# Kernel tuning notes

Hardware: AMD Instinct MI355X
Metric: run time of the kernel (lower is better)

## Reference

```python
import jax, jax.numpy as jnp
import numpy as np

B, S, HID, NH = 4, 1024, 1024, 16
HD = HID // NH  # 64


def setup_inputs() -> dict:
    key = jax.random.key(0)
    ks = jax.random.split(key, 8)
    scale = 0.02
    return {
        "attention_mask": jnp.zeros((B, 1, 1, S), dtype=jnp.float32),
        "query": jax.random.normal(ks[0], (B, S, HID), dtype=jnp.float32),
        "key": jax.random.normal(ks[1], (B, S, HID), dtype=jnp.float32),
        "value": jax.random.normal(ks[2], (B, S, HID), dtype=jnp.float32),
        "Wq": jax.random.normal(ks[3], (HID, HID), dtype=jnp.float32) * scale,
        "bq": jnp.zeros((HID,), dtype=jnp.float32),
        "Wk": jax.random.normal(ks[4], (HID, HID), dtype=jnp.float32) * scale,
        "bk": jnp.zeros((HID,), dtype=jnp.float32),
    }


def reference(attention_mask, query, key, value, Wq, bq, Wk, bk):
    # Linear projections (torch Linear: x @ W.T + b)
    q = query @ Wq.T + bq  # [B,S,HID]
    k = key @ Wk.T + bk    # [B,S,HID]
    # split heads -> [B,NH,S,HD]
    q = q.reshape(B, S, NH, HD).transpose(0, 2, 1, 3)
    k = k.reshape(B, S, NH, HD).transpose(0, 2, 1, 3)
    scores = jnp.einsum("bhqd,bhkd->bhqk", q, k) / jnp.sqrt(jnp.float32(HD))
    scores = scores + attention_mask  # additive mask broadcast [B,1,1,S]
    probs = jax.nn.softmax(scores, axis=-1)  # [B,NH,S,S]
    # V is shared across heads; head-mean folds into a single contraction:
    # mean_h(probs_h @ V) = (sum_h probs_h) @ V / NH
    out = jnp.einsum("bhqk,bkv->bqv", probs, value) / NH  # [B,S,HID]
    return out
```

## Files before the change

kernel.cpp:

```cpp
#include <hip/hip_runtime.h>
#include <hip/hip_bf16.h>
#include <hip/hip_fp16.h>

#define B_    4
#define S_    1024
#define HID_  1024
#define NH_   16
#define HD_   64

typedef _Float16 half8 __attribute__((ext_vector_type(8)));
typedef _Float16 half4v __attribute__((ext_vector_type(4)));
typedef float f32x4 __attribute__((ext_vector_type(4)));

#define LOG2E 1.44269504f

__device__ __forceinline__ void gload_lds16(const void* g, void* l) {
    __builtin_amdgcn_global_load_lds(
        (const __attribute__((address_space(1))) unsigned int*)g,
        (__attribute__((address_space(3))) unsigned int*)l, 16, 0, 0);
}

__global__ __launch_bounds__(256) void pack_qkw(
    const float* __restrict__ s0, _Float16* __restrict__ d0, int n40,
    const float* __restrict__ s1, _Float16* __restrict__ d1, int n41,
    const float* __restrict__ s2, _Float16* __restrict__ d2, int n42,
    const float* __restrict__ s3, _Float16* __restrict__ d3, int n43)
{
    int y = blockIdx.y;
    const float* s = y == 0 ? s0 : y == 1 ? s1 : y == 2 ? s2 : s3;
    _Float16*    d = y == 0 ? d0 : y == 1 ? d1 : y == 2 ? d2 : d3;
    int n4         = y == 0 ? n40 : y == 1 ? n41 : y == 2 ? n42 : n43;
    int i = blockIdx.x * 256 + threadIdx.x;
    if (i >= n4) return;
    float4 v = ((const float4*)s)[i];
    half4v h;
    h[0] = (_Float16)v.x; h[1] = (_Float16)v.y;
    h[2] = (_Float16)v.z; h[3] = (_Float16)v.w;
    ((half4v*)d)[i] = h;
}

__global__ __launch_bounds__(256) void vt_combine(
    const _Float16* __restrict__ P, _Float16* __restrict__ o,
    const float* __restrict__ V, _Float16* __restrict__ Vt)
{
    __shared__ float t[32][33];
    if (blockIdx.y == 0) {
        if (blockIdx.x >= 2048) return;
        const long QS = (long)B_ * S_ * S_;
        long i = (long)(blockIdx.x * 256 + threadIdx.x) * 8;
        half8 a = *(const half8*)(P + i);
        half8 b = *(const half8*)(P + QS + i);
        half8 c = *(const half8*)(P + 2 * QS + i);
        half8 d = *(const half8*)(P + 3 * QS + i);
        half8 r;
#pragma unroll
        for (int e = 0; e < 8; e++)
            r[e] = (_Float16)((float)a[e] + (float)b[e] + (float)c[e] + (float)d[e]);
        *(half8*)(o + i) = r;
    } else {
        const int x  = blockIdx.x;
        const int b  = x >> 10;
        const int s0 = ((x >> 5) & 31) * 32;
        const int h0 = (x & 31) * 32;
        const int tx = threadIdx.x & 31, ty = threadIdx.x >> 5;
#pragma unroll
        for (int rr = 0; rr < 4; rr++) {
            int s = s0 + ty + rr * 8;
            t[ty + rr * 8][tx] = V[((long)b * S_ + s) * HID_ + h0 + tx];
        }
        __syncthreads();
#pragma unroll
        for (int rr = 0; rr < 4; rr++) {
            int h = h0 + ty + rr * 8;
            Vt[((long)b * HID_ + h) * S_ + s0 + tx] = (_Float16)t[tx][ty + rr * 8];
        }
    }
}

__global__ __launch_bounds__(512) void proj_qk_f16(
    const _Float16* __restrict__ Aq, const _Float16* __restrict__ Wqh,
    const float* __restrict__ bq_, _Float16* __restrict__ Oq,
    const _Float16* __restrict__ Ak, const _Float16* __restrict__ Wkh,
    const float* __restrict__ bk_, _Float16* __restrict__ Ok)
{
    const _Float16* A  = blockIdx.z ? Ak : Aq;
    const _Float16* Bm = blockIdx.z ? Wkh : Wqh;
    const float* bias  = blockIdx.z ? bk_ : bq_;
    _Float16* Co       = blockIdx.z ? Ok : Oq;

    __shared__ _Float16 Al[128 * 32];
    __shared__ _Float16 Bl[128 * 32];

    const int tid  = threadIdx.x;
    const int wv   = tid >> 6;
    const int lane = tid & 63;
    const int l15  = lane & 15;
    const int quad = lane >> 4;
    const int wm   = wv & 1, wn = wv >> 1;
    const int m0   = blockIdx.y * 128, n0 = blockIdx.x * 128;
    const int sr   = tid >> 2;
    const int sc   = (tid & 3) * 8;

    f32x4 acc[4][2];
#pragma unroll
    for (int i = 0; i < 4; i++)
#pragma unroll
        for (int j = 0; j < 2; j++) acc[i][j] = (f32x4){0.f, 0.f, 0.f, 0.f};

    for (int kt = 0; kt < HID_; kt += 32) {
        gload_lds16(A  + (long)(m0 + sr) * HID_ + kt + sc, Al + (long)tid * 8);
        gload_lds16(Bm + (long)(n0 + sr) * HID_ + kt + sc, Bl + (long)tid * 8);
        __syncthreads();

        half8 af[4], bfm[2];
#pragma unroll
        for (int i = 0; i < 4; i++)
            af[i] = *(const half8*)(Al + (wm * 64 + i * 16 + l15) * 32 + quad * 8);
#pragma unroll
        for (int j = 0; j < 2; j++)
            bfm[j] = *(const half8*)(Bl + (wn * 32 + j * 16 + l15) * 32 + quad * 8);
#pragma unroll
        for (int i = 0; i < 4; i++)
#pragma unroll
            for (int j = 0; j < 2; j++)
                acc[i][j] = __builtin_amdgcn_mfma_f32_16x16x32_f16(
                    af[i], bfm[j], acc[i][j], 0, 0, 0);
        __syncthreads();
    }

#pragma unroll
    for (int j = 0; j < 2; j++) {
        int col = n0 + wn * 32 + j * 16 + l15;
        float bv = bias[col];
        int h = col >> 6, d = col & 63;
#pragma unroll
        for (int i = 0; i < 4; i++) {
            int row = m0 + wm * 64 + i * 16 + quad * 4;
            int bb = row >> 10, ss = row & 1023;
#pragma unroll
            for (int r = 0; r < 4; r++)
                Co[((long)(bb * NH_ + h) * S_ + ss + r) * HD_ + d] =
                    (_Float16)(acc[i][j][r] + bv);
        }
    }
}

__global__ __launch_bounds__(512) void attn_psum_f16(
    const _Float16* __restrict__ qb,
    const _Float16* __restrict__ kb,
    const float* __restrict__ mask,
    _Float16* __restrict__ P)
{
    const int b    = blockIdx.y;
    const int q0   = blockIdx.x * 16;
    const int hz   = blockIdx.z;
    const int tid  = threadIdx.x;
    const int w    = tid >> 6;
    const int lane = tid & 63;
    const int l15  = lane & 15;
    const int quad = lane >> 4;

    __shared__ float redS[2][16][8];

    const float SC = 0.125f * LOG2E;

    float mreg[8];
#pragma unroll
    for (int t = 0; t < 8; t++)
        mreg[t] = mask[b * S_ + t * 128 + w * 16 + l15] * LOG2E;

    f32x4 acc[8];
#pragma unroll
    for (int t = 0; t < 8; t++) acc[t] = (f32x4){0.f, 0.f, 0.f, 0.f};

    for (int ii = 0; ii < 4; ii++) {
        const int h = hz * 4 + ii;
        const _Float16* qh = qb + ((long)(b * NH_ + h) * S_) * HD_;
        const _Float16* kh = kb + ((long)(b * NH_ + h) * S_) * HD_;

        half8 a0 = *(const half8*)(qh + (long)(q0 + l15) * HD_ + quad * 8);
        half8 a1 = *(const half8*)(qh + (long)(q0 + l15) * HD_ + 32 + quad * 8);

        f32x4 s[8];
#pragma unroll
        for (int cc = 0; cc < 8; cc++) {
            const _Float16* kp =
                kh + (long)(cc * 128 + w * 16 + l15) * HD_ + quad * 8;
            half8 b0 = *(const half8*)kp;
            half8 b1 = *(const half8*)(kp + 32);
            f32x4 c = (f32x4){0.f, 0.f, 0.f, 0.f};
            c = __builtin_amdgcn_mfma_f32_16x16x32_f16(a0, b0, c, 0, 0, 0);
            c = __builtin_amdgcn_mfma_f32_16x16x32_f16(a1, b1, c, 0, 0, 0);
            s[cc] = c;
        }

        const int p = ii & 1;
        float sm[4] = {0.f, 0.f, 0.f, 0.f};
#pragma unroll
        for (int t = 0; t < 8; t++)
#pragma unroll
            for (int r = 0; r < 4; r++) {
                float pr = exp2f(s[t][r] * SC + mreg[t]);
                s[t][r] = pr;
                sm[r] += pr;
            }
#pragma unroll
        for (int off = 1; off < 16; off <<= 1)
#pragma unroll
            for (int r = 0; r < 4; r++) sm[r] += __shfl_xor(sm[r], off);
        if (l15 == 0)
#pragma unroll
            for (int r = 0; r < 4; r++) redS[p][quad * 4 + r][w] = sm[r];
        __syncthreads();

#pragma unroll
        for (int r = 0; r < 4; r++) {
            float4 v0 = *(float4*)&redS[p][quad * 4 + r][0];
            float4 v1 = *(float4*)&redS[p][quad * 4 + r][4];
            float tot = (v0.x + v0.y + v0.z + v0.w) + (v1.x + v1.y + v1.z + v1.w);
            float inv = 1.f / tot;
#pragma unroll
            for (int t = 0; t < 8; t++) acc[t][r] += s[t][r] * inv;
        }
    }

    _Float16* prow = P + (long)hz * ((long)B_ * S_ * S_) + (long)(b * S_ + q0) * S_;
#pragma unroll
    for (int t = 0; t < 8; t++)
#pragma unroll
        for (int r = 0; r < 4; r++) {
            int row = quad * 4 + r;
            prow[(long)row * S_ + t * 128 + w * 16 + l15] = (_Float16)acc[t][r];
        }
}

__global__ __launch_bounds__(256) void pv_f16(
    const _Float16* __restrict__ Pc,
    const _Float16* __restrict__ Vt,
    float* __restrict__ out)
{
    const int b = blockIdx.z;
    const _Float16* A  = Pc + (long)b * S_ * S_;
    const _Float16* Bm = Vt + (long)b * HID_ * S_;

    __shared__ _Float16 Al[128 * 32];
    __shared__ _Float16 Bl[64 * 32];

    const int tid  = threadIdx.x;
    const int wv   = tid >> 6;
    const int lane = tid & 63;
    const int l15  = lane & 15;
    const int quad = lane >> 4;
    const int wm   = wv & 1, wn = wv >> 1;
    const int m0   = blockIdx.y * 128, n0 = blockIdx.x * 64;
    const int sr   = tid >> 2;
    const int sc   = (tid & 3) * 8;

    f32x4 acc[4][2];
#pragma unroll
    for (int i = 0; i < 4; i++)
#pragma unroll
        for (int j = 0; j < 2; j++) acc[i][j] = (f32x4){0.f, 0.f, 0.f, 0.f};

    for (int kt = 0; kt < S_; kt += 32) {
        gload_lds16(A  + (long)(m0 + sr) * S_ + kt + sc,      Al + (long)tid * 8);
        gload_lds16(A  + (long)(m0 + 64 + sr) * S_ + kt + sc, Al + (long)(256 + tid) * 8);
        gload_lds16(Bm + (long)(n0 + sr) * S_ + kt + sc,      Bl + (long)tid * 8);
        __syncthreads();

        half8 af[4], bfm[2];
#pragma unroll
        for (int i = 0; i < 4; i++)
            af[i] = *(const half8*)(Al + (wm * 64 + i * 16 + l15) * 32 + quad * 8);
#pragma unroll
        for (int j = 0; j < 2; j++)
            bfm[j] = *(const half8*)(Bl + (wn * 32 + j * 16 + l15) * 32 + quad * 8);
#pragma unroll
        for (int i = 0; i < 4; i++)
#pragma unroll
            for (int j = 0; j < 2; j++)
                acc[i][j] = __builtin_amdgcn_mfma_f32_16x16x32_f16(
                    af[i], bfm[j], acc[i][j], 0, 0, 0);
        __syncthreads();
    }

    const float alpha = 1.f / NH_;
#pragma unroll
    for (int i = 0; i < 4; i++) {
        int row = m0 + wm * 64 + i * 16 + quad * 4;
#pragma unroll
        for (int j = 0; j < 2; j++) {
            int col = n0 + wn * 32 + j * 16 + l15;
#pragma unroll
            for (int r = 0; r < 4; r++)
                out[(long)(b * S_ + row + r) * HID_ + col] = acc[i][j][r] * alpha;
        }
    }
}

extern "C" void kernel_launch(void* const* d_in, const int* in_sizes, int n_in,
                              void* d_out, int out_size, void* d_ws, size_t ws_size,
                              hipStream_t stream)
{
    const float* mask  = (const float*)d_in[0];
    const float* query = (const float*)d_in[1];
    const float* key   = (const float*)d_in[2];
    const float* value = (const float*)d_in[3];
    const float* Wq    = (const float*)d_in[4];
    const float* bq    = (const float*)d_in[5];
    const float* Wk    = (const float*)d_in[6];
    const float* bk    = (const float*)d_in[7];
    float* out = (float*)d_out;

    char* ws = (char*)d_ws;
    const long MB = 1l << 20;
    _Float16* qbuf = (_Float16*)(ws);
    _Float16* kbuf = (_Float16*)(ws + 8 * MB);
    _Float16* qh   = (_Float16*)(ws + 16 * MB);
    _Float16* kh   = (_Float16*)(ws + 24 * MB);
    _Float16* Wqh  = (_Float16*)(ws + 32 * MB);
    _Float16* Wkh  = (_Float16*)(ws + 34 * MB);
    _Float16* Pq   = (_Float16*)(ws + 16 * MB);
    _Float16* Vt   = (_Float16*)(ws);
    _Float16* psum = (_Float16*)(ws + 8 * MB);

    const int nQK = (B_ * S_ * HID_) / 4;
    const int nW  = (HID_ * HID_) / 4;

    pack_qkw<<<dim3(nQK / 256, 4), dim3(256), 0, stream>>>(
        query, qh, nQK, key, kh, nQK, Wq, Wqh, nW, Wk, Wkh, nW);

    proj_qk_f16<<<dim3(HID_ / 128, (B_ * S_) / 128, 2), dim3(512), 0, stream>>>(
        qh, Wqh, bq, qbuf, kh, Wkh, bk, kbuf);

    attn_psum_f16<<<dim3(S_ / 16, B_, 4), dim3(512), 0, stream>>>(
        qbuf, kbuf, mask, Pq);

    vt_combine<<<dim3(4096, 2), dim3(256), 0, stream>>>(Pq, psum, value, Vt);

    pv_f16<<<dim3(HID_ / 64, S_ / 128, B_), dim3(256), 0, stream>>>(psum, Vt, out);
}
```

Measured before the change: 244.1 us.

## Fuse fp32-to-fp16 conversion into projection GEMM and re-layout Q/K for attention

Removes the separate pack kernel by having the projection GEMM load fp32 query/key/weights directly, convert them to fp16 in registers and store them into padded LDS tiles. The Q and K outputs are written in blocked layouts so the attention kernel's MFMA fragment loads become contiguous 16-byte reads. The PV GEMM switches from direct global-to-LDS loads to register staging with a padded stride, issuing global loads before the barrier so they overlap the previous tile's compute. This drops a full read-write pass over the inputs and weights, but the GEMMs now convert in the inner loop and use register staging instead of the async LDS load path.

```diff
diff --git a/kernel.cpp b/kernel.cpp
--- a/kernel.cpp
+++ b/kernel.cpp
@@ -1,5 +1,4 @@
 #include <hip/hip_runtime.h>
-#include <hip/hip_bf16.h>
 #include <hip/hip_fp16.h>
 
 #define B_    4
@@ -8,11 +7,20 @@
 #define NH_   16
 #define HD_   64
 
+#define LOG2E 1.44269504f
+#define PSTR  40
+
 typedef _Float16 half8 __attribute__((ext_vector_type(8)));
-typedef _Float16 half4v __attribute__((ext_vector_type(4)));
 typedef float f32x4 __attribute__((ext_vector_type(4)));
 
-#define LOG2E 1.44269504f
+__device__ __forceinline__ half8 cvt8(float4 a, float4 b) {
+    half8 h;
+    h[0] = (_Float16)a.x; h[1] = (_Float16)a.y;
+    h[2] = (_Float16)a.z; h[3] = (_Float16)a.w;
+    h[4] = (_Float16)b.x; h[5] = (_Float16)b.y;
+    h[6] = (_Float16)b.z; h[7] = (_Float16)b.w;
+    return h;
+}
 
 __device__ __forceinline__ void gload_lds16(const void* g, void* l) {
     __builtin_amdgcn_global_load_lds(
@@ -20,23 +28,171 @@
         (__attribute__((address_space(3))) unsigned int*)l, 16, 0, 0);
 }
 
-__global__ __launch_bounds__(256) void pack_qkw(
-    const float* __restrict__ s0, _Float16* __restrict__ d0, int n40,
-    const float* __restrict__ s1, _Float16* __restrict__ d1, int n41,
-    const float* __restrict__ s2, _Float16* __restrict__ d2, int n42,
-    const float* __restrict__ s3, _Float16* __restrict__ d3, int n43)
-{
-    int y = blockIdx.y;
-    const float* s = y == 0 ? s0 : y == 1 ? s1 : y == 2 ? s2 : s3;
-    _Float16*    d = y == 0 ? d0 : y == 1 ? d1 : y == 2 ? d2 : d3;
-    int n4         = y == 0 ? n40 : y == 1 ? n41 : y == 2 ? n42 : n43;
-    int i = blockIdx.x * 256 + threadIdx.x;
-    if (i >= n4) return;
-    float4 v = ((const float4*)s)[i];
-    half4v h;
-    h[0] = (_Float16)v.x; h[1] = (_Float16)v.y;
-    h[2] = (_Float16)v.z; h[3] = (_Float16)v.w;
-    ((half4v*)d)[i] = h;
+__global__ __launch_bounds__(512) void proj_qk_f16(
+    const float* __restrict__ query, const float* __restrict__ Wq,
+    const float* __restrict__ bq, _Float16* __restrict__ Oq,
+    const float* __restrict__ key, const float* __restrict__ Wk,
+    const float* __restrict__ bk, _Float16* __restrict__ Ok)
+{
+    const float* A    = blockIdx.z ? key : query;
+    const float* Wm   = blockIdx.z ? Wk  : Wq;
+    const float* bias = blockIdx.z ? bk  : bq;
+    _Float16* Co      = blockIdx.z ? Ok  : Oq;
+
+    __shared__ _Float16 Al[128 * PSTR];
+    __shared__ _Float16 Bl[128 * PSTR];
+
+    const int tid  = threadIdx.x;
+    const int wv   = tid >> 6;
+    const int lane = tid & 63;
+    const int l15  = lane & 15;
+    const int quad = lane >> 4;
+    const int wm   = wv & 1, wn = wv >> 1;
+    const int m0   = blockIdx.y * 128, n0 = blockIdx.x * 128;
+    const int sr   = tid >> 2;
+    const int sc   = (tid & 3) * 8;
+
+    f32x4 acc[4][2];
+#pragma unroll
+    for (int i = 0; i < 4; i++)
+#pragma unroll
+        for (int j = 0; j < 2; j++) acc[i][j] = (f32x4){0.f, 0.f, 0.f, 0.f};
+
+    for (int kt = 0; kt < HID_; kt += 32) {
+        const float* ap = A  + (long)(m0 + sr) * HID_ + kt + sc;
+        const float* bp = Wm + (long)(n0 + sr) * HID_ + kt + sc;
+        float4 av0 = *(const float4*)ap, av1 = *(const float4*)(ap + 4);
+        float4 bv0 = *(const float4*)bp, bv1 = *(const float4*)(bp + 4);
+        __syncthreads();
+        *(half8*)(Al + sr * PSTR + sc) = cvt8(av0, av1);
+        *(half8*)(Bl + sr * PSTR + sc) = cvt8(bv0, bv1);
+        __syncthreads();
+
+        half8 af[4], bfm[2];
+#pragma unroll
+        for (int i = 0; i < 4; i++)
+            af[i] = *(const half8*)(Al + (wm * 64 + i * 16 + l15) * PSTR + quad * 8);
+#pragma unroll
+        for (int j = 0; j < 2; j++)
+            bfm[j] = *(const half8*)(Bl + (wn * 32 + j * 16 + l15) * PSTR + quad * 8);
+#pragma unroll
+        for (int i = 0; i < 4; i++)
+#pragma unroll
+            for (int j = 0; j < 2; j++)
+                acc[i][j] = __builtin_amdgcn_mfma_f32_16x16x32_f16(
+                    af[i], bfm[j], acc[i][j], 0, 0, 0);
+    }
+
+    const int isQ = (blockIdx.z == 0);
+#pragma unroll
+    for (int j = 0; j < 2; j++) {
+        int col = n0 + wn * 32 + j * 16 + l15;
+        float bv = bias[col];
+        int h = col >> 6, d = col & 63, p = d >> 3, jj = d & 7;
+#pragma unroll
+        for (int i = 0; i < 4; i++) {
+            int row = m0 + wm * 64 + i * 16 + quad * 4;
+            int bb = row >> 10, ss = row & 1023;
+            long base;
+            if (isQ)
+                base = ((((long)(bb * NH_ + h) * 64 + (ss >> 4)) * 8 + p) * 16
+                        + (ss & 15)) * 8 + jj;
+            else
+                base = (((long)(bb * NH_ + h) * 8 + p) * 1024 + ss) * 8 + jj;
+#pragma unroll
+            for (int r = 0; r < 4; r++)
+                Co[base + r * 8] = (_Float16)(acc[i][j][r] + bv);
+        }
+    }
+}
+
+__global__ __launch_bounds__(512) void attn_psum_f16(
+    const _Float16* __restrict__ qb,
+    const _Float16* __restrict__ kb,
+    const float* __restrict__ mask,
+    _Float16* __restrict__ P)
+{
+    const int b    = blockIdx.y;
+    const int qt   = blockIdx.x;
+    const int q0   = qt * 16;
+    const int hz   = blockIdx.z;
+    const int tid  = threadIdx.x;
+    const int w    = tid >> 6;
+    const int lane = tid & 63;
+    const int l15  = lane & 15;
+    const int quad = lane >> 4;
+
+    __shared__ float redS[2][16][8];
+
+    const float SC = 0.125f * LOG2E;
+
+    float mreg[8];
+#pragma unroll
+    for (int t = 0; t < 8; t++)
+        mreg[t] = mask[b * S_ + t * 128 + w * 16 + l15] * LOG2E;
+
+    f32x4 acc[8];
+#pragma unroll
+    for (int t = 0; t < 8; t++) acc[t] = (f32x4){0.f, 0.f, 0.f, 0.f};
+
+    for (int ii = 0; ii < 4; ii++) {
+        const int h = hz * 4 + ii;
+        const _Float16* qh = qb + ((long)(b * NH_ + h) * 64 + qt) * 1024;
+        const _Float16* kh = kb + (long)(b * NH_ + h) * 8192 * 8;
+
+        half8 a0 = *(const half8*)(qh + quad * 128 + l15 * 8);
+        half8 a1 = *(const half8*)(qh + (quad + 4) * 128 + l15 * 8);
+
+        f32x4 s[8];
+#pragma unroll
+        for (int cc = 0; cc < 8; cc++) {
+            const int key = cc * 128 + w * 16 + l15;
+            half8 b0 = *(const half8*)(kh + (long)quad * 8192 + key * 8);
+            half8 b1 = *(const half8*)(kh + (long)(quad + 4) * 8192 + key * 8);
+            f32x4 c = (f32x4){0.f, 0.f, 0.f, 0.f};
+            c = __builtin_amdgcn_mfma_f32_16x16x32_f16(a0, b0, c, 0, 0, 0);
+            c = __builtin_amdgcn_mfma_f32_16x16x32_f16(a1, b1, c, 0, 0, 0);
+            s[cc] = c;
+        }
+
+        const int p = ii & 1;
+        float sm[4] = {0.f, 0.f, 0.f, 0.f};
+#pragma unroll
+        for (int t = 0; t < 8; t++)
+#pragma unroll
+            for (int r = 0; r < 4; r++) {
+                float pr = exp2f(s[t][r] * SC + mreg[t]);
+                s[t][r] = pr;
+                sm[r] += pr;
+            }
+#pragma unroll
+        for (int off = 1; off < 16; off <<= 1)
+#pragma unroll
+            for (int r = 0; r < 4; r++) sm[r] += __shfl_xor(sm[r], off);
+        if (l15 == 0)
+#pragma unroll
+            for (int r = 0; r < 4; r++) redS[p][quad * 4 + r][w] = sm[r];
+        __syncthreads();
+
+#pragma unroll
+        for (int r = 0; r < 4; r++) {
+            float4 v0 = *(float4*)&redS[p][quad * 4 + r][0];
+            float4 v1 = *(float4*)&redS[p][quad * 4 + r][4];
+            float tot = (v0.x + v0.y + v0.z + v0.w) + (v1.x + v1.y + v1.z + v1.w);
+            float inv = 1.f / tot;
+#pragma unroll
+            for (int t = 0; t < 8; t++) acc[t][r] += s[t][r] * inv;
+        }
+    }
+
+    _Float16* prow = P + (long)hz * ((long)B_ * S_ * S_) + (long)(b * S_ + q0) * S_;
+#pragma unroll
+    for (int t = 0; t < 8; t++)
+#pragma unroll
+        for (int r = 0; r < 4; r++) {
+            int row = quad * 4 + r;
+            prow[(long)row * S_ + t * 128 + w * 16 + l15] = (_Float16)acc[t][r];
+        }
 }
 
 __global__ __launch_bounds__(256) void vt_combine(
@@ -77,163 +233,6 @@
     }
 }
 
-__global__ __launch_bounds__(512) void proj_qk_f16(
-    const _Float16* __restrict__ Aq, const _Float16* __restrict__ Wqh,
-    const float* __restrict__ bq_, _Float16* __restrict__ Oq,
-    const _Float16* __restrict__ Ak, const _Float16* __restrict__ Wkh,
-    const float* __restrict__ bk_, _Float16* __restrict__ Ok)
-{
-    const _Float16* A  = blockIdx.z ? Ak : Aq;
-    const _Float16* Bm = blockIdx.z ? Wkh : Wqh;
-    const float* bias  = blockIdx.z ? bk_ : bq_;
-    _Float16* Co       = blockIdx.z ? Ok : Oq;
-
-    __shared__ _Float16 Al[128 * 32];
-    __shared__ _Float16 Bl[128 * 32];
-
-    const int tid  = threadIdx.x;
-    const int wv   = tid >> 6;
-    const int lane = tid & 63;
-    const int l15  = lane & 15;
-    const int quad = lane >> 4;
-    const int wm   = wv & 1, wn = wv >> 1;
-    const int m0   = blockIdx.y * 128, n0 = blockIdx.x * 128;
-    const int sr   = tid >> 2;
-    const int sc   = (tid & 3) * 8;
-
-    f32x4 acc[4][2];
-#pragma unroll
-    for (int i = 0; i < 4; i++)
-#pragma unroll
-        for (int j = 0; j < 2; j++) acc[i][j] = (f32x4){0.f, 0.f, 0.f, 0.f};
-
-    for (int kt = 0; kt < HID_; kt += 32) {
-        gload_lds16(A  + (long)(m0 + sr) * HID_ + kt + sc, Al + (long)tid * 8);
-        gload_lds16(Bm + (long)(n0 + sr) * HID_ + kt + sc, Bl + (long)tid * 8);
-        __syncthreads();
-
-        half8 af[4], bfm[2];
-#pragma unroll
-        for (int i = 0; i < 4; i++)
-            af[i] = *(const half8*)(Al + (wm * 64 + i * 16 + l15) * 32 + quad * 8);
-#pragma unroll
-        for (int j = 0; j < 2; j++)
-            bfm[j] = *(const half8*)(Bl + (wn * 32 + j * 16 + l15) * 32 + quad * 8);
-#pragma unroll
-        for (int i = 0; i < 4; i++)
-#pragma unroll
-            for (int j = 0; j < 2; j++)
-                acc[i][j] = __builtin_amdgcn_mfma_f32_16x16x32_f16(
-                    af[i], bfm[j], acc[i][j], 0, 0, 0);
-        __syncthreads();
-    }
-
-#pragma unroll
-    for (int j = 0; j < 2; j++) {
-        int col = n0 + wn * 32 + j * 16 + l15;
-        float bv = bias[col];
-        int h = col >> 6, d = col & 63;
-#pragma unroll
-        for (int i = 0; i < 4; i++) {
-            int row = m0 + wm * 64 + i * 16 + quad * 4;
-            int bb = row >> 10, ss = row & 1023;
-#pragma unroll
-            for (int r = 0; r < 4; r++)
-                Co[((long)(bb * NH_ + h) * S_ + ss + r) * HD_ + d] =
-                    (_Float16)(acc[i][j][r] + bv);
-        }
-    }
-}
-
-__global__ __launch_bounds__(512) void attn_psum_f16(
-    const _Float16* __restrict__ qb,
-    const _Float16* __restrict__ kb,
-    const float* __restrict__ mask,
-    _Float16* __restrict__ P)
-{
-    const int b    = blockIdx.y;
-    const int q0   = blockIdx.x * 16;
-    const int hz   = blockIdx.z;
-    const int tid  = threadIdx.x;
-    const int w    = tid >> 6;
-    const int lane = tid & 63;
-    const int l15  = lane & 15;
-    const int quad = lane >> 4;
-
-    __shared__ float redS[2][16][8];
-
-    const float SC = 0.125f * LOG2E;
-
-    float mreg[8];
-#pragma unroll
-    for (int t = 0; t < 8; t++)
-        mreg[t] = mask[b * S_ + t * 128 + w * 16 + l15] * LOG2E;
-
-    f32x4 acc[8];
-#pragma unroll
-    for (int t = 0; t < 8; t++) acc[t] = (f32x4){0.f, 0.f, 0.f, 0.f};
-
-    for (int ii = 0; ii < 4; ii++) {
-        const int h = hz * 4 + ii;
-        const _Float16* qh = qb + ((long)(b * NH_ + h) * S_) * HD_;
-        const _Float16* kh = kb + ((long)(b * NH_ + h) * S_) * HD_;
-
-        half8 a0 = *(const half8*)(qh + (long)(q0 + l15) * HD_ + quad * 8);
-        half8 a1 = *(const half8*)(qh + (long)(q0 + l15) * HD_ + 32 + quad * 8);
-
-        f32x4 s[8];
-#pragma unroll
-        for (int cc = 0; cc < 8; cc++) {
-            const _Float16* kp =
-                kh + (long)(cc * 128 + w * 16 + l15) * HD_ + quad * 8;
-            half8 b0 = *(const half8*)kp;
-            half8 b1 = *(const half8*)(kp + 32);
-            f32x4 c = (f32x4){0.f, 0.f, 0.f, 0.f};
-            c = __builtin_amdgcn_mfma_f32_16x16x32_f16(a0, b0, c, 0, 0, 0);
-            c = __builtin_amdgcn_mfma_f32_16x16x32_f16(a1, b1, c, 0, 0, 0);
-            s[cc] = c;
-        }
-
-        const int p = ii & 1;
-        float sm[4] = {0.f, 0.f, 0.f, 0.f};
-#pragma unroll
-        for (int t = 0; t < 8; t++)
-#pragma unroll
-            for (int r = 0; r < 4; r++) {
-                float pr = exp2f(s[t][r] * SC + mreg[t]);
-                s[t][r] = pr;
-                sm[r] += pr;
-            }
-#pragma unroll
-        for (int off = 1; off < 16; off <<= 1)
-#pragma unroll
-            for (int r = 0; r < 4; r++) sm[r] += __shfl_xor(sm[r], off);
-        if (l15 == 0)
-#pragma unroll
-            for (int r = 0; r < 4; r++) redS[p][quad * 4 + r][w] = sm[r];
-        __syncthreads();
-
-#pragma unroll
-        for (int r = 0; r < 4; r++) {
-            float4 v0 = *(float4*)&redS[p][quad * 4 + r][0];
-            float4 v1 = *(float4*)&redS[p][quad * 4 + r][4];
-            float tot = (v0.x + v0.y + v0.z + v0.w) + (v1.x + v1.y + v1.z + v1.w);
-            float inv = 1.f / tot;
-#pragma unroll
-            for (int t = 0; t < 8; t++) acc[t][r] += s[t][r] * inv;
-        }
-    }
-
-    _Float16* prow = P + (long)hz * ((long)B_ * S_ * S_) + (long)(b * S_ + q0) * S_;
-#pragma unroll
-    for (int t = 0; t < 8; t++)
-#pragma unroll
-        for (int r = 0; r < 4; r++) {
-            int row = quad * 4 + r;
-            prow[(long)row * S_ + t * 128 + w * 16 + l15] = (_Float16)acc[t][r];
-        }
-}
-
 __global__ __launch_bounds__(256) void pv_f16(
     const _Float16* __restrict__ Pc,
     const _Float16* __restrict__ Vt,
@@ -243,8 +242,8 @@
     const _Float16* A  = Pc + (long)b * S_ * S_;
     const _Float16* Bm = Vt + (long)b * HID_ * S_;
 
-    __shared__ _Float16 Al[128 * 32];
-    __shared__ _Float16 Bl[64 * 32];
+    __shared__ _Float16 Al[128 * PSTR];
+    __shared__ _Float16 Bl[64 * PSTR];
 
     const int tid  = threadIdx.x;
     const int wv   = tid >> 6;
@@ -263,25 +262,28 @@
         for (int j = 0; j < 2; j++) acc[i][j] = (f32x4){0.f, 0.f, 0.f, 0.f};
 
     for (int kt = 0; kt < S_; kt += 32) {
-        gload_lds16(A  + (long)(m0 + sr) * S_ + kt + sc,      Al + (long)tid * 8);
-        gload_lds16(A  + (long)(m0 + 64 + sr) * S_ + kt + sc, Al + (long)(256 + tid) * 8);
-        gload_lds16(Bm + (long)(n0 + sr) * S_ + kt + sc,      Bl + (long)tid * 8);
+        half8 a0 = *(const half8*)(A  + (long)(m0 + sr) * S_ + kt + sc);
+        half8 a1 = *(const half8*)(A  + (long)(m0 + 64 + sr) * S_ + kt + sc);
+        half8 b0 = *(const half8*)(Bm + (long)(n0 + sr) * S_ + kt + sc);
+        __syncthreads();
+        *(half8*)(Al + sr * PSTR + sc) = a0;
+        *(half8*)(Al + (64 + sr) * PSTR + sc) = a1;
+        *(half8*)(Bl + sr * PSTR + sc) = b0;
         __syncthreads();
 
         half8 af[4], bfm[2];
 #pragma unroll
         for (int i = 0; i < 4; i++)
-            af[i] = *(const half8*)(Al + (wm * 64 + i * 16 + l15) * 32 + quad * 8);
+            af[i] = *(const half8*)(Al + (wm * 64 + i * 16 + l15) * PSTR + quad * 8);
 #pragma unroll
         for (int j = 0; j < 2; j++)
-            bfm[j] = *(const half8*)(Bl + (wn * 32 + j * 16 + l15) * 32 + quad * 8);
+            bfm[j] = *(const half8*)(Bl + (wn * 32 + j * 16 + l15) * PSTR + quad * 8);
 #pragma unroll
         for (int i = 0; i < 4; i++)
 #pragma unroll
             for (int j = 0; j < 2; j++)
                 acc[i][j] = __builtin_amdgcn_mfma_f32_16x16x32_f16(
                     af[i], bfm[j], acc[i][j], 0, 0, 0);
-        __syncthreads();
     }
 
     const float alpha = 1.f / NH_;
@@ -316,22 +318,12 @@
     const long MB = 1l << 20;
     _Float16* qbuf = (_Float16*)(ws);
     _Float16* kbuf = (_Float16*)(ws + 8 * MB);
-    _Float16* qh   = (_Float16*)(ws + 16 * MB);
-    _Float16* kh   = (_Float16*)(ws + 24 * MB);
-    _Float16* Wqh  = (_Float16*)(ws + 32 * MB);
-    _Float16* Wkh  = (_Float16*)(ws + 34 * MB);
     _Float16* Pq   = (_Float16*)(ws + 16 * MB);
     _Float16* Vt   = (_Float16*)(ws);
     _Float16* psum = (_Float16*)(ws + 8 * MB);
 
-    const int nQK = (B_ * S_ * HID_) / 4;
-    const int nW  = (HID_ * HID_) / 4;
-
-    pack_qkw<<<dim3(nQK / 256, 4), dim3(256), 0, stream>>>(
-        query, qh, nQK, key, kh, nQK, Wq, Wqh, nW, Wk, Wkh, nW);
-
     proj_qk_f16<<<dim3(HID_ / 128, (B_ * S_) / 128, 2), dim3(512), 0, stream>>>(
-        qh, Wqh, bq, qbuf, kh, Wkh, bk, kbuf);
+        query, Wq, bq, qbuf, key, Wk, bk, kbuf);
 
     attn_psum_f16<<<dim3(S_ / 16, B_, 4), dim3(512), 0, stream>>>(
         qbuf, kbuf, mask, Pq);
```

Result: faster. 215.9 us (-11.6%).
